# Kernel tuning notes

Hardware: AMD Instinct MI355X
Metric: run time of the kernel (lower is better)

Reference implementation:

```python
import jax, jax.numpy as jnp
import numpy as np

IN_CH = 512; OUT_CH = 512; NOISE_SIZE = 512; K = 3; A = 0.2
B = 4; H = 32
_G = float(np.sqrt(2.0 / (1.0 + A * A)))                 # leaky_relu gain, a=0.2
CONV_SCALE = _G / float(np.sqrt(IN_CH * K * K))          # equal-lr kaiming scale (fan_in = in_ch*3*3)
MS_SCALE = float(np.sqrt(2.0 / (NOISE_SIZE + IN_CH)))    # equal-lr xavier scale on make_s linear
RGB_SCALE = _G * float(np.sqrt(2.0 / (OUT_CH + 3)))      # equal-lr xavier scale on 1x1 to_rgb


def upsample2x(x):
    # torch F.interpolate(scale_factor=2, mode='bilinear', align_corners=False)
    b, c, h, w = x.shape
    return jax.image.resize(x, (b, c, 2 * h, 2 * w), method='bilinear')


def mod_conv(x, style, weight, bias, ms_w, ms_b, w_scale, demodulate, pad):
    # style -> per-sample input-channel scales s: (B, Cin)
    s = style @ (ms_w.T * MS_SCALE) + ms_b
    Wmod = (weight * w_scale)[None] * s[:, None, :, None, None]   # (B, Cout, Cin, k, k)
    if demodulate:
        d = jax.lax.rsqrt(jnp.sum(Wmod * Wmod, axis=(2, 3, 4)) + 1e-8)
        Wmod = Wmod * d[:, :, None, None, None]
    conv1 = lambda xi, wi: jax.lax.conv_general_dilated(
        xi[None], wi, (1, 1), [(pad, pad), (pad, pad)],
        dimension_numbers=('NCHW', 'OIHW', 'NCHW'))[0]
    y = jax.vmap(conv1)(x, Wmod)                                   # per-sample weights == grouped conv
    return y + bias[None, :, None, None]


def lrelu(x):
    return jnp.where(x >= 0, x, A * x)


def setup_inputs() -> dict:
    key = jax.random.key(0)
    ks = jax.random.split(key, 19)
    r = lambda i, shape: jax.random.normal(ks[i], shape, dtype=jnp.float32)
    return {
        'maps': r(0, (B, IN_CH, H, H)),
        'w': r(1, (B, NOISE_SIZE)),
        'rgb': r(2, (B, 3, H, H)),
        'noise0': r(3, (B, 1, 2 * H, 2 * H)),
        'noise1': r(4, (B, 1, 2 * H, 2 * H)),
        'conv0_w': r(5, (OUT_CH, IN_CH, K, K)),
        'conv0_b': 0.1 * r(6, (OUT_CH,)),
        'ms0_w': r(7, (IN_CH, NOISE_SIZE)),
        'ms0_b': jnp.ones((IN_CH,), jnp.float32),
        'ns0': 0.1 * r(8, (OUT_CH,)),
        'conv1_w': r(9, (OUT_CH, OUT_CH, K, K)),
        'conv1_b': 0.1 * r(10, (OUT_CH,)),
        'ms1_w': r(11, (OUT_CH, NOISE_SIZE)),
        'ms1_b': jnp.ones((OUT_CH,), jnp.float32),
        'ns1': 0.1 * r(12, (OUT_CH,)),
        'rgb_w': r(13, (3, OUT_CH, 1, 1)),
        'rgb_b': 0.1 * r(14, (3,)),
        'msr_w': r(15, (OUT_CH, NOISE_SIZE)),
        'msr_b': jnp.ones((OUT_CH,), jnp.float32),
    }


def reference(maps, w, rgb, noise0, noise1,
              conv0_w, conv0_b, ms0_w, ms0_b, ns0,
              conv1_w, conv1_b, ms1_w, ms1_b, ns1,
              rgb_w, rgb_b, msr_w, msr_b):
    # upsample branch (upsample=True)
    rgb = upsample2x(rgb)
    maps = upsample2x(maps)
    # layer 0: modulated conv -> noise -> leaky relu
    h = mod_conv(maps, w, conv0_w, conv0_b, ms0_w, ms0_b, CONV_SCALE, True, 1)
    h = lrelu(h + ns0[None, :, None, None] * noise0)
    # layer 1
    h = mod_conv(h, w, conv1_w, conv1_b, ms1_w, ms1_b, CONV_SCALE, True, 1)
    h = lrelu(h + ns1[None, :, None, None] * noise1)
    # to_rgb: 1x1 modulated conv, no demodulation
    rgb_out = rgb + mod_conv(h, w, rgb_w, rgb_b, msr_w, msr_b, RGB_SCALE, False, 0)
    return (rgb_out, h)
```

## Files before the change

kernel.cpp:

```cpp
#include <hip/hip_runtime.h>
#include <stdint.h>


#define BATCH 4
#define CH 512
#define NPP 4356
#define HOUT_OFF 49152

static constexpr double G_GAIN = 1.3867504905630728;
static constexpr float CONV_SCALE_F = (float)(G_GAIN / 67.88225099390857);
static constexpr float MS_SCALE_F = 0.044194173824159216f;
static constexpr float RGB_SCALE_F = (float)(G_GAIN * 1.4142135623730951 / 22.693611435820433);

typedef __attribute__((ext_vector_type(8))) short short8;
typedef __attribute__((ext_vector_type(4))) float floatx4;

#define OFF_FLAG   0
#define OFF_S0     256
#define OFF_S1     (OFF_S0 + 8192)
#define OFF_SR     (OFF_S1 + 8192)
#define OFF_D0     (OFF_SR + 8192)
#define OFF_D1     (OFF_D0 + 8192)
#define OFF_B0F    (OFF_D1 + 8192)
#define OFF_B1F    (OFF_B0F + 2048)
#define OFF_NS0F   (OFF_B1F + 2048)
#define OFF_NS1F   (OFF_NS0F + 2048)
#define OFF_RGBBF  (OFF_NS1F + 2048)
#define OFF_WMODR  (OFF_RGBBF + 256)
#define OFF_N0F    (OFF_WMODR + 24576)
#define OFF_N1F    (OFF_N0F + 65536)
#define OFF_WT0    (OFF_N1F + 65536)
#define WT_BYTES   4718592
#define OFF_WT1    (OFF_WT0 + WT_BYTES)
#define OFF_XP0    (OFF_WT1 + WT_BYTES)
#define XP_BYTES   17842176
#define OFF_XP1    (OFF_XP0 + XP_BYTES)

__device__ __forceinline__ float bf2f(unsigned short u) {
  return __uint_as_float(((unsigned int)u) << 16);
}
__device__ __forceinline__ unsigned short f2bf(float f) {
  unsigned int x = __float_as_uint(f);
  unsigned int r = x + 0x7FFFu + ((x >> 16) & 1u);
  return (unsigned short)(r >> 16);
}
__device__ __forceinline__ float ldin(const void* p, long i, int bf) {
  if (bf) return bf2f(((const unsigned short*)p)[i]);
  return ((const float*)p)[i];
}
__device__ __forceinline__ void async_ld16(const void* g, void* l) {
  __builtin_amdgcn_global_load_lds(
      (const __attribute__((address_space(1))) unsigned int*)g,
      (__attribute__((address_space(3))) unsigned int*)l, 16, 0, 0);
}
__device__ __forceinline__ void upw(int o, int n_in, int& lo, int& hi, float& wlo) {
  int k = o >> 1;
  if (o & 1) { lo = k; hi = k + 1; if (hi > n_in - 1) hi = n_in - 1; wlo = 0.75f; }
  else       { lo = k - 1; if (lo < 0) lo = 0; hi = k; wlo = 0.25f; }
}

__global__ void k_flag(const unsigned int* msb, int* flag) {
  if (threadIdx.x == 0 && blockIdx.x == 0)
    *flag = (msb[0] == 0x3F803F80u) ? 1 : 0;
}

__global__ void k_styles(const void* w, const void* msw0, const void* msb0,
                         const void* msw1, const void* msb1,
                         const void* mswr, const void* msbr,
                         float* s0, float* s1, float* sr, const int* flagp) {
  const int bf = *flagp;
  const int mat = blockIdx.x >> 7, chunk = blockIdx.x & 127;
  const int wv = threadIdx.x >> 6, lane = threadIdx.x & 63;
  const int i = chunk * 4 + wv;
  const void* msw; const void* msb; float* out;
  if (mat == 0)      { msw = msw0; msb = msb0; out = s0; }
  else if (mat == 1) { msw = msw1; msb = msb1; out = s1; }
  else               { msw = mswr; msb = msbr; out = sr; }
  float a[4] = {0.f, 0.f, 0.f, 0.f};
  const int n0 = lane * 8;
  if (bf) {
    short8 m8 = *(const short8*)((const unsigned short*)msw + (long)i * 512 + n0);
    for (int b = 0; b < 4; ++b) {
      short8 w8 = *(const short8*)((const unsigned short*)w + b * 512 + n0);
      float s = 0.f;
      for (int e = 0; e < 8; ++e)
        s += bf2f((unsigned short)m8[e]) * bf2f((unsigned short)w8[e]);
      a[b] = s;
    }
  } else {
    const float* mrow = (const float*)msw + (long)i * 512 + n0;
    float4 m0v = *(const float4*)mrow, m1v = *(const float4*)(mrow + 4);
    for (int b = 0; b < 4; ++b) {
      const float* wr = (const float*)w + b * 512 + n0;
      float4 w0v = *(const float4*)wr, w1v = *(const float4*)(wr + 4);
      a[b] = m0v.x * w0v.x + m0v.y * w0v.y + m0v.z * w0v.z + m0v.w * w0v.w +
             m1v.x * w1v.x + m1v.y * w1v.y + m1v.z * w1v.z + m1v.w * w1v.w;
    }
  }
  for (int off = 1; off < 64; off <<= 1)
    for (int b = 0; b < 4; ++b) a[b] += __shfl_xor(a[b], off, 64);
  if (lane == 0) {
    const float mb = ldin(msb, i, bf);
    for (int b = 0; b < 4; ++b) out[b * 512 + i] = a[b] * MS_SCALE_F + mb;
  }
}

__global__ void k_convert(const void* b0, const void* b1, const void* nv0, const void* nv1,
                          const void* rb, const void* rw, const void* noise0, const void* noise1,
                          float* ob0, float* ob1, float* ons0, float* ons1, float* orb,
                          float* owmr, float* on0, float* on1,
                          const float* sr, const int* flagp) {
  const int bf = *flagp;
  const int t = blockIdx.x * blockDim.x + threadIdx.x;
  const int stride = gridDim.x * blockDim.x;
  if (t < 512) {
    ob0[t] = ldin(b0, t, bf); ob1[t] = ldin(b1, t, bf);
    ons0[t] = ldin(nv0, t, bf); ons1[t] = ldin(nv1, t, bf);
  }
  if (t < 3) orb[t] = ldin(rb, t, bf);
  for (int i = t; i < 16384; i += stride) {
    on0[i] = ldin(noise0, i, bf);
    on1[i] = ldin(noise1, i, bf);
  }
  for (int i = t; i < 4 * 3 * 512; i += stride) {
    int b = i / 1536; int r = i - b * 1536; int c = r >> 9; int ci = r & 511;
    owmr[i] = RGB_SCALE_F * ldin(rw, c * 512 + ci, bf) * sr[b * 512 + ci];
  }
}

__global__ void k_wtd(const void* w0, const void* w1, const float* s0, const float* s1,
                      unsigned short* Wt0, unsigned short* Wt1,
                      float* S0, float* S1, const int* flagp) {
  const int bf = *flagp;
  const int l = blockIdx.x >> 9, co = blockIdx.x & 511;
  const void* w = l ? w1 : w0;
  const float* s = l ? s1 : s0;
  unsigned short* Wt = l ? Wt1 : Wt0;
  float* S = l ? S1 : S0;
  float part[4] = {0.f, 0.f, 0.f, 0.f};
  for (int h = 0; h < 2; ++h) {
    const int ci = threadIdx.x + h * 256;
    const int kb = ci >> 5, q = (ci >> 3) & 3, j = ci & 7;
    const long rbase = ((long)co * 512 + ci) * 9;
    float wsq = 0.f;
    for (int t = 0; t < 9; ++t) {
      float v = ldin(w, rbase + t, bf);
      wsq += v * v;
      Wt[((((long)t * 16 + kb) * 4 + q) * 512 + co) * 8 + j] = f2bf(v);
    }
    for (int b = 0; b < 4; ++b) {
      float sv = s[b * 512 + ci];
      part[b] += sv * sv * wsq;
    }
  }
  __shared__ float red[256 * 4];
  for (int b = 0; b < 4; ++b) red[threadIdx.x * 4 + b] = part[b];
  __syncthreads();
  for (int off = 128; off > 0; off >>= 1) {
    if (threadIdx.x < off)
      for (int b = 0; b < 4; ++b)
        red[threadIdx.x * 4 + b] += red[(threadIdx.x + off) * 4 + b];
    __syncthreads();
  }
  if (threadIdx.x < 4) S[threadIdx.x * 512 + co] = red[threadIdx.x];
}

__global__ void k_upt(const void* maps, const float* s0, unsigned short* Xp0,
                      const int* flagp) {
  const int bf = *flagp;
  const int t = blockIdx.x, kb = blockIdx.y, b = blockIdx.z;
  __shared__ float lds[32][4][32];
  {
    const int ciq = threadIdx.x >> 5;
    const int x = threadIdx.x & 31;
    for (int cc = 0; cc < 4; ++cc) {
      const int ci = cc * 8 + ciq;
      const long cbase = ((long)(b * 512 + kb * 32 + ci)) << 10;
      for (int r = 0; r < 4; ++r) {
        int ir = 2 * t - 1 + r;
        ir = ir < 0 ? 0 : (ir > 31 ? 31 : ir);
        lds[ci][r][x] = ldin(maps, cbase + ir * 32 + x, bf);
      }
    }
  }
  __syncthreads();
  const int q = threadIdx.x >> 6, px = threadIdx.x & 63;
  int xlo, xhi; float wx;
  upw(px, 32, xlo, xhi, wx);
  float sv[8];
  for (int jj = 0; jj < 8; ++jj) sv[jj] = s0[b * 512 + kb * 32 + q * 8 + jj];
  for (int y = 0; y < 4; ++y) {
    const int yg = 4 * t + y;
    int ylo, yhi; float wy;
    upw(yg, 32, ylo, yhi, wy);
    const int rlo = ylo - (2 * t - 1), rhi = yhi - (2 * t - 1);
    short8 pk;
    for (int jj = 0; jj < 8; ++jj) {
      const int ci = q * 8 + jj;
      float vlo = wx * lds[ci][rlo][xlo] + (1.f - wx) * lds[ci][rlo][xhi];
      float vhi = wx * lds[ci][rhi][xlo] + (1.f - wx) * lds[ci][rhi][xhi];
      float v = (wy * vlo + (1.f - wy) * vhi) * sv[jj];
      pk[jj] = (short)f2bf(v);
    }
    *(short8*)&Xp0[((((long)b * 16 + kb) * 4 + q) * NPP + (yg + 1) * 66 + (px + 1)) * 8] = pk;
  }
}

#define MFMA16 __builtin_amdgcn_mfma_f32_16x16x32_bf16
template <int LAYER>
__global__ __launch_bounds__(256, 2) void k_conv(
    const unsigned short* __restrict__ Wt,
    const unsigned short* Xp,
    const float* __restrict__ Ssum,
    const float* __restrict__ bias,
    const float* __restrict__ nsc,
    const float* __restrict__ noise,
    const float* __restrict__ snext,
    unsigned short* XpOut,
    void* dout,
    const int* __restrict__ flagp) {
  __shared__ __align__(16) unsigned short Al[12288];
  __shared__ __align__(16) unsigned short Bl[8448];
  const int mt = blockIdx.x & 3, nt = blockIdx.x >> 2, b = blockIdx.y;
  const int m0 = mt << 7, y0 = nt << 1;
  const int lane = threadIdx.x & 63, wv = threadIdx.x >> 6;
  const int wm = wv >> 1, wn = wv & 1;
  const int q = lane >> 4, l15 = lane & 15;

  const floatx4 vz = {0.f, 0.f, 0.f, 0.f};
  floatx4 c00 = vz, c01 = vz, c02 = vz, c03 = vz;
  floatx4 c10 = vz, c11 = vz, c12 = vz, c13 = vz;
  floatx4 c20 = vz, c21 = vz, c22 = vz, c23 = vz;
  floatx4 c30 = vz, c31 = vz, c32 = vz, c33 = vz;

  const int q1 = wv >> 1, hh = wv & 1;
  const unsigned short* Ard = Al + ((q * 3) * 128 + wm * 64 + l15) * 8;
  const unsigned short* Brd = Bl + ((q * 4 + wn) * 66 + l15) * 8;

#pragma unroll 1
  for (int kb = 0; kb < 16; ++kb) {
    for (int ky = 0; ky < 3; ++ky) {
      __syncthreads();
      for (int s = 0; s < 6; ++s) {
        const int kx = s >> 1;
        const int qq = q1 + ((s & 1) << 1);
        const unsigned short* src =
            Wt + ((((long)(ky * 3 + kx) * 16 + kb) * 4 + qq) * 512 + m0 + hh * 64 + lane) * 8;
        unsigned short* dst = Al + ((qq * 3 + kx) * 128 + hh * 64) * 8;
        async_ld16(src, dst);
      }
      if (ky == 0) {
        for (int r = 0; r < 4; ++r) {
          const unsigned short* src =
              Xp + ((((long)b * 16 + kb) * 4 + wv) * NPP + (y0 + r) * 66) * 8 + lane * 8;
          unsigned short* dst = Bl + ((wv * 4 + r) * 66) * 8;
          async_ld16(src, dst);
          if (lane < 2) async_ld16(src + 512, dst + 512);
        }
      }
      __syncthreads();
#define TAPC(KX)                                                               \
  {                                                                            \
    const unsigned short* ap = Ard + (KX)*1024;                                \
    const unsigned short* bp = Brd + (ky * 66 + (KX)) * 8;                     \
    short8 aa0 = *(const short8*)(ap);                                         \
    short8 aa1 = *(const short8*)(ap + 128);                                   \
    short8 aa2 = *(const short8*)(ap + 256);                                   \
    short8 aa3 = *(const short8*)(ap + 384);                                   \
    short8 bb0 = *(const short8*)(bp);                                         \
    short8 bb1 = *(const short8*)(bp + 128);                                   \
    short8 bb2 = *(const short8*)(bp + 256);                                   \
    short8 bb3 = *(const short8*)(bp + 384);                                   \
    c00 = MFMA16(aa0, bb0, c00, 0, 0, 0); c01 = MFMA16(aa0, bb1, c01, 0, 0, 0);\
    c02 = MFMA16(aa0, bb2, c02, 0, 0, 0); c03 = MFMA16(aa0, bb3, c03, 0, 0, 0);\
    c10 = MFMA16(aa1, bb0, c10, 0, 0, 0); c11 = MFMA16(aa1, bb1, c11, 0, 0, 0);\
    c12 = MFMA16(aa1, bb2, c12, 0, 0, 0); c13 = MFMA16(aa1, bb3, c13, 0, 0, 0);\
    c20 = MFMA16(aa2, bb0, c20, 0, 0, 0); c21 = MFMA16(aa2, bb1, c21, 0, 0, 0);\
    c22 = MFMA16(aa2, bb2, c22, 0, 0, 0); c23 = MFMA16(aa2, bb3, c23, 0, 0, 0);\
    c30 = MFMA16(aa3, bb0, c30, 0, 0, 0); c31 = MFMA16(aa3, bb1, c31, 0, 0, 0);\
    c32 = MFMA16(aa3, bb2, c32, 0, 0, 0); c33 = MFMA16(aa3, bb3, c33, 0, 0, 0);\
  }
      TAPC(0)
      TAPC(1)
      TAPC(2)
#undef TAPC
    }
  }

  floatx4 accv[4][4] = {{c00, c01, c02, c03}, {c10, c11, c12, c13},
                        {c20, c21, c22, c23}, {c30, c31, c32, c33}};
  const int bfflag = *flagp;
  const int coB = m0 + (wm << 6) + ((lane >> 4) << 2);
  const int xB = lane & 15;
  const int y = y0 + wn;
  for (int i = 0; i < 4; ++i) {
    const int co = coB + (i << 4);
    float Ds[4], bi[4], nv[4], sx[4];
    for (int r = 0; r < 4; ++r) {
      float Sv = Ssum[b * 512 + co + r];
      Ds[r] = CONV_SCALE_F * rsqrtf(CONV_SCALE_F * CONV_SCALE_F * Sv + 1e-8f);
      bi[r] = bias[co + r];
      nv[r] = nsc[co + r];
      sx[r] = (LAYER == 0) ? snext[b * 512 + co + r] : 0.f;
    }
    for (int j = 0; j < 4; ++j) {
      const int x = (j << 4) + xB;
      const int p = (y << 6) + x;
      const float nz = noise[b * 4096 + p];
      if (LAYER == 0) {
        unsigned long long pk = 0ull;
        for (int r = 0; r < 4; ++r) {
          float v = accv[i][j][r] * Ds[r] + bi[r] + nv[r] * nz;
          v = (v >= 0.f) ? v : 0.2f * v;
          pk |= (unsigned long long)f2bf(v * sx[r]) << (16 * r);
        }
        const int pp = (y + 1) * 66 + (x + 1);
        const long o = ((((long)b * 16 + (co >> 5)) * 4 + ((co >> 3) & 3)) * NPP + pp) * 8 + (co & 7);
        *(unsigned long long*)(XpOut + o) = pk;
      } else {
        for (int r = 0; r < 4; ++r) {
          float v = accv[i][j][r] * Ds[r] + bi[r] + nv[r] * nz;
          v = (v >= 0.f) ? v : 0.2f * v;
          const long o = (((long)(b * 512 + co + r)) << 12) + p;
          if (bfflag) ((unsigned short*)dout)[HOUT_OFF + o] = f2bf(v);
          else        ((float*)dout)[HOUT_OFF + o] = v;
        }
      }
    }
  }
}

__global__ void k_rgb(const void* rgb_in, const float* wmodr, const float* rgbb,
                      void* dout, const int* flagp) {
  const int bf = *flagp;
  const int b = blockIdx.y, p0 = blockIdx.x * 64;
  const int px = threadIdx.x & 63, g = threadIdx.x >> 6;
  const char* hbytes = (const char*)dout + (long)HOUT_OFF * (bf ? 2 : 4);
  float a0 = 0.f, a1 = 0.f, a2 = 0.f;
  const float* wm = wmodr + b * 1536;
  for (int ci = g * 128; ci < g * 128 + 128; ++ci) {
    const long o = (((long)(b * 512 + ci)) << 12) + p0 + px;
    const float hv = bf ? bf2f(((const unsigned short*)hbytes)[o])
                        : ((const float*)hbytes)[o];
    a0 += wm[ci] * hv;
    a1 += wm[512 + ci] * hv;
    a2 += wm[1024 + ci] * hv;
  }
  __shared__ float red[4][3][64];
  red[g][0][px] = a0; red[g][1][px] = a1; red[g][2][px] = a2;
  __syncthreads();
  if (g == 0) {
    const int p = p0 + px;
    const int y = p >> 6, x = p & 63;
    int ylo, yhi, xlo, xhi; float wy, wx;
    upw(y, 32, ylo, yhi, wy);
    upw(x, 32, xlo, xhi, wx);
    for (int c = 0; c < 3; ++c) {
      float s = red[0][c][px] + red[1][c][px] + red[2][c][px] + red[3][c][px];
      const long base = (long)(b * 3 + c) << 10;
      const float v00 = ldin(rgb_in, base + ylo * 32 + xlo, bf);
      const float v01 = ldin(rgb_in, base + ylo * 32 + xhi, bf);
      const float v10 = ldin(rgb_in, base + yhi * 32 + xlo, bf);
      const float v11 = ldin(rgb_in, base + yhi * 32 + xhi, bf);
      const float up = wy * (wx * v00 + (1.f - wx) * v01) +
                       (1.f - wy) * (wx * v10 + (1.f - wx) * v11);
      const float v = up + s + rgbb[c];
      const long o = ((long)(b * 3 + c) << 12) + p;
      if (bf) ((unsigned short*)dout)[o] = f2bf(v);
      else    ((float*)dout)[o] = v;
    }
  }
}

extern "C" void kernel_launch(void* const* d_in, const int* in_sizes, int n_in,
                              void* d_out, int out_size, void* d_ws, size_t ws_size,
                              hipStream_t stream) {
  char* ws = (char*)d_ws;
  int* flag = (int*)(ws + OFF_FLAG);
  float* s0 = (float*)(ws + OFF_S0);
  float* s1 = (float*)(ws + OFF_S1);
  float* sr = (float*)(ws + OFF_SR);
  float* S0 = (float*)(ws + OFF_D0);
  float* S1 = (float*)(ws + OFF_D1);
  float* b0f = (float*)(ws + OFF_B0F);
  float* b1f = (float*)(ws + OFF_B1F);
  float* ns0f = (float*)(ws + OFF_NS0F);
  float* ns1f = (float*)(ws + OFF_NS1F);
  float* rgbbf = (float*)(ws + OFF_RGBBF);
  float* wmodr = (float*)(ws + OFF_WMODR);
  float* n0f = (float*)(ws + OFF_N0F);
  float* n1f = (float*)(ws + OFF_N1F);
  unsigned short* Wt0 = (unsigned short*)(ws + OFF_WT0);
  unsigned short* Wt1 = (unsigned short*)(ws + OFF_WT1);
  unsigned short* Xp0 = (unsigned short*)(ws + OFF_XP0);
  unsigned short* Xp1 = (unsigned short*)(ws + OFF_XP1);

  k_flag<<<1, 64, 0, stream>>>((const unsigned int*)d_in[8], flag);
  hipMemsetAsync(Xp0, 0, 2 * XP_BYTES, stream);
  k_styles<<<384, 256, 0, stream>>>(d_in[1], d_in[7], d_in[8], d_in[12], d_in[13],
                                    d_in[17], d_in[18], s0, s1, sr, flag);
  k_convert<<<64, 256, 0, stream>>>(d_in[6], d_in[11], d_in[9], d_in[14], d_in[16],
                                    d_in[15], d_in[3], d_in[4], b0f, b1f, ns0f, ns1f,
                                    rgbbf, wmodr, n0f, n1f, sr, flag);
  k_wtd<<<1024, 256, 0, stream>>>(d_in[5], d_in[10], s0, s1, Wt0, Wt1, S0, S1, flag);
  k_upt<<<dim3(16, 16, 4), 256, 0, stream>>>(d_in[0], s0, Xp0, flag);
  k_conv<0><<<dim3(128, 4), 256, 0, stream>>>(Wt0, Xp0, S0, b0f, ns0f, n0f, s1, Xp1,
                                              d_out, flag);
  k_conv<1><<<dim3(128, 4), 256, 0, stream>>>(Wt1, Xp1, S1, b1f, ns1f, n1f, s1, Xp1,
                                              d_out, flag);
  k_rgb<<<dim3(64, 4), 256, 0, stream>>>(d_in[2], wmodr, rgbbf, d_out, flag);
  (void)in_sizes; (void)n_in; (void)out_size; (void)ws_size;
}
```

Baseline: 312.3 us.

## Double-buffer conv weight tiles and prefetch next stage with a single barrier

The conv kernel now keeps two LDS buffers for the weight tile. It issues async loads for the next (kb, ky) stage before computing the current one, so each iteration needs one barrier instead of two. Input rows are fetched two at a time into a smaller tile without the padded columns, and the left and right zero-padding is applied in registers when the B fragments are read. The full-buffer memset is replaced by a small kernel that zeroes only the top and bottom padding rows. This adds index arithmetic and selects in the inner loop, and correctness depends on the async loads being complete at the single barrier.

```diff
diff --git a/kernel.cpp b/kernel.cpp
--- a/kernel.cpp
+++ b/kernel.cpp
@@ -62,6 +62,16 @@
 __global__ void k_flag(const unsigned int* msb, int* flag) {
   if (threadIdx.x == 0 && blockIdx.x == 0)
     *flag = (msb[0] == 0x3F803F80u) ? 1 : 0;
+}
+
+__global__ void k_zero(unsigned short* Xp) {
+  const int idx = blockIdx.x * 256 + threadIdx.x;
+  const int plane = idx / 132;
+  const int rem = idx - plane * 132;
+  const int row65 = rem >= 66;
+  const int col = rem - (row65 ? 66 : 0);
+  const short8 z = {0, 0, 0, 0, 0, 0, 0, 0};
+  *(short8*)&Xp[((long)plane * NPP + (row65 ? 65 : 0) * 66 + col) * 8] = z;
 }
 
 __global__ void k_styles(const void* w, const void* msw0, const void* msb0,
@@ -219,13 +229,14 @@
     unsigned short* XpOut,
     void* dout,
     const int* __restrict__ flagp) {
-  __shared__ __align__(16) unsigned short Al[12288];
-  __shared__ __align__(16) unsigned short Bl[8448];
+  __shared__ __align__(16) unsigned short Al[2][12288];
+  __shared__ __align__(16) unsigned short Bl[8192];
   const int mt = blockIdx.x & 3, nt = blockIdx.x >> 2, b = blockIdx.y;
   const int m0 = mt << 7, y0 = nt << 1;
   const int lane = threadIdx.x & 63, wv = threadIdx.x >> 6;
   const int wm = wv >> 1, wn = wv & 1;
   const int q = lane >> 4, l15 = lane & 15;
+  const int q1 = wv >> 1, hh = wv & 1;
 
   const floatx4 vz = {0.f, 0.f, 0.f, 0.f};
   floatx4 c00 = vz, c01 = vz, c02 = vz, c03 = vz;
@@ -233,44 +244,64 @@
   floatx4 c20 = vz, c21 = vz, c22 = vz, c23 = vz;
   floatx4 c30 = vz, c31 = vz, c32 = vz, c33 = vz;
 
-  const int q1 = wv >> 1, hh = wv & 1;
-  const unsigned short* Ard = Al + ((q * 3) * 128 + wm * 64 + l15) * 8;
-  const unsigned short* Brd = Bl + ((q * 4 + wn) * 66 + l15) * 8;
-
+  auto issueA = [&](int kb, int ky, int bu) {
+    for (int s = 0; s < 6; ++s) {
+      const int kx = s >> 1;
+      const int qq = q1 + ((s & 1) << 1);
+      const unsigned short* src =
+          Wt + ((((long)(ky * 3 + kx) * 16 + kb) * 4 + qq) * 512 + m0 + hh * 64 + lane) * 8;
+      async_ld16(src, &Al[bu][((qq * 3 + kx) * 128 + hh * 64) * 8]);
+    }
+  };
+  auto issueB2 = [&](int kb, int r0) {
+    for (int r = 0; r < 2; ++r) {
+      const int row = r0 + r;
+      const unsigned short* src =
+          Xp + ((((long)b * 16 + kb) * 4 + wv) * NPP + (long)(y0 + row) * 66 + 1 + lane) * 8;
+      async_ld16(src, &Bl[((row * 4 + wv) * 64) * 8]);
+    }
+  };
+
+  issueA(0, 0, 0);
+  issueB2(0, 0);
+
+  const short8 z8 = {0, 0, 0, 0, 0, 0, 0, 0};
+  int buf = 0;
 #pragma unroll 1
   for (int kb = 0; kb < 16; ++kb) {
     for (int ky = 0; ky < 3; ++ky) {
       __syncthreads();
-      for (int s = 0; s < 6; ++s) {
-        const int kx = s >> 1;
-        const int qq = q1 + ((s & 1) << 1);
-        const unsigned short* src =
-            Wt + ((((long)(ky * 3 + kx) * 16 + kb) * 4 + qq) * 512 + m0 + hh * 64 + lane) * 8;
-        unsigned short* dst = Al + ((qq * 3 + kx) * 128 + hh * 64) * 8;
-        async_ld16(src, dst);
+      {
+        int kyn = ky + 1, kbn = kb;
+        if (kyn == 3) { kyn = 0; kbn = kb + 1; if (kbn == 16) kbn = 0; }
+        issueA(kbn, kyn, buf ^ 1);
+        if (ky == 0) issueB2(kb, 2);
+        else if (ky == 2) issueB2(kb + 1 == 16 ? 0 : kb + 1, 0);
       }
-      if (ky == 0) {
-        for (int r = 0; r < 4; ++r) {
-          const unsigned short* src =
-              Xp + ((((long)b * 16 + kb) * 4 + wv) * NPP + (y0 + r) * 66) * 8 + lane * 8;
-          unsigned short* dst = Bl + ((wv * 4 + r) * 66) * 8;
-          async_ld16(src, dst);
-          if (lane < 2) async_ld16(src + 512, dst + 512);
-        }
-      }
-      __syncthreads();
+      const unsigned short* Ab = &Al[buf][0];
+      const int sq = ((wn + ky) * 4 + q) * 64;
 #define TAPC(KX)                                                               \
   {                                                                            \
-    const unsigned short* ap = Ard + (KX)*1024;                                \
-    const unsigned short* bp = Brd + (ky * 66 + (KX)) * 8;                     \
+    const unsigned short* ap = Ab + ((q * 3 + (KX)) * 128 + wm * 64 + l15) * 8;\
     short8 aa0 = *(const short8*)(ap);                                         \
     short8 aa1 = *(const short8*)(ap + 128);                                   \
     short8 aa2 = *(const short8*)(ap + 256);                                   \
     short8 aa3 = *(const short8*)(ap + 384);                                   \
-    short8 bb0 = *(const short8*)(bp);                                         \
-    short8 bb1 = *(const short8*)(bp + 128);                                   \
-    short8 bb2 = *(const short8*)(bp + 256);                                   \
-    short8 bb3 = *(const short8*)(bp + 384);                                   \
+    short8 bb0, bb1, bb2, bb3;                                                 \
+    {                                                                          \
+      int p = 0 * 16 + l15 + (KX);                                             \
+      int pc = p < 1 ? 0 : p - 1;                                              \
+      bb0 = *(const short8*)&Bl[(sq + pc) * 8];                                \
+      if ((KX) == 0) bb0 = (p == 0) ? z8 : bb0;                                \
+    }                                                                          \
+    bb1 = *(const short8*)&Bl[(sq + 1 * 16 + l15 + (KX)-1) * 8];               \
+    bb2 = *(const short8*)&Bl[(sq + 2 * 16 + l15 + (KX)-1) * 8];               \
+    {                                                                          \
+      int p = 3 * 16 + l15 + (KX);                                             \
+      int pc = p > 64 ? 63 : p - 1;                                            \
+      bb3 = *(const short8*)&Bl[(sq + pc) * 8];                                \
+      if ((KX) == 2) bb3 = (p == 65) ? z8 : bb3;                               \
+    }                                                                          \
     c00 = MFMA16(aa0, bb0, c00, 0, 0, 0); c01 = MFMA16(aa0, bb1, c01, 0, 0, 0);\
     c02 = MFMA16(aa0, bb2, c02, 0, 0, 0); c03 = MFMA16(aa0, bb3, c03, 0, 0, 0);\
     c10 = MFMA16(aa1, bb0, c10, 0, 0, 0); c11 = MFMA16(aa1, bb1, c11, 0, 0, 0);\
@@ -284,6 +315,7 @@
       TAPC(1)
       TAPC(2)
 #undef TAPC
+      buf ^= 1;
     }
   }
 
@@ -396,7 +428,7 @@
   unsigned short* Xp1 = (unsigned short*)(ws + OFF_XP1);
 
   k_flag<<<1, 64, 0, stream>>>((const unsigned int*)d_in[8], flag);
-  hipMemsetAsync(Xp0, 0, 2 * XP_BYTES, stream);
+  k_zero<<<264, 256, 0, stream>>>(Xp0);
   k_styles<<<384, 256, 0, stream>>>(d_in[1], d_in[7], d_in[8], d_in[12], d_in[13],
                                     d_in[17], d_in[18], s0, s1, sr, flag);
   k_convert<<<64, 256, 0, stream>>>(d_in[6], d_in[11], d_in[9], d_in[14], d_in[16],
```

New measurement: 308.9 us. About the same (-1.1%).
